# Kernel tuning notes

Hardware: AMD Instinct MI355X
Metric: run time of the kernel (lower is better)

## Reference

```python
import jax, jax.numpy as jnp
import numpy as np

HEADS = 4
DIM_HEAD = 128
HIDDEN = HEADS * DIM_HEAD  # 512
DIM = 256
EMBED = 256


def mish(x):
    return x * jnp.tanh(jax.nn.softplus(x))


def setup_inputs() -> dict:
    key = jax.random.key(0)
    k = jax.random.split(key, 7)
    b, a, f, t = 64, 8, DIM, 256
    x = jax.random.normal(k[0], (b, a, f, t), dtype=jnp.float32)
    time = jax.random.normal(k[1], (b, a, EMBED), dtype=jnp.float32)
    # to_qkv: Conv2d(dim, 3*hidden, 1, bias=False) -> weight [3*hidden, dim]
    w_qkv = jax.random.normal(k[2], (3 * HIDDEN, DIM), dtype=jnp.float32) * (1.0 / np.sqrt(DIM))
    # time_mlp: Mish -> Linear(embed, 3*hidden)
    w_time = jax.random.normal(k[3], (3 * HIDDEN, EMBED), dtype=jnp.float32) * (1.0 / np.sqrt(EMBED))
    b_time = jax.random.normal(k[4], (3 * HIDDEN,), dtype=jnp.float32) * 0.01
    # to_out: Conv2d(hidden, dim, 1) with bias
    w_out = jax.random.normal(k[5], (DIM, HIDDEN), dtype=jnp.float32) * (1.0 / np.sqrt(HIDDEN))
    b_out = jax.random.normal(k[6], (DIM,), dtype=jnp.float32) * 0.01
    return {"x": x, "time": time, "w_qkv": w_qkv, "w_time": w_time,
            "b_time": b_time, "w_out": w_out, "b_out": b_out}


def reference(x, time, w_qkv, w_time, b_time, w_out, b_out):
    b, a, f, t = x.shape
    heads, c = HEADS, DIM_HEAD
    # x: b a f t -> b f a t (channels-first for 1x1 conv)
    xp = jnp.transpose(x, (0, 2, 1, 3))  # [b, f, a, t]
    # 1x1 conv == channel GEMM
    qkv = jnp.einsum('of,bfat->boat', w_qkv, xp)  # [b, 3*hidden, a, t]
    # time MLP: Mish -> Linear; bias broadcast over t
    temb = mish(time) @ w_time.T + b_time          # [b, a, 3*hidden]
    temb = jnp.transpose(temb, (0, 2, 1))[..., None]  # [b, 3*hidden, a, 1]
    qkv = qkv + temb
    # 'b (qkv heads c) h w -> qkv (b h) heads c w' with h=a, w=t
    qkv = qkv.reshape(b, 3, heads, c, a, t)
    qkv = jnp.transpose(qkv, (1, 0, 4, 2, 3, 5)).reshape(3, b * a, heads, c, t)
    q, k, v = qkv[0], qkv[1], qkv[2]  # each [(b a), heads, c, t]
    k = jax.nn.softmax(k, axis=-1)
    # linear attention: context over keys/values, then apply to q
    context = jnp.einsum('bhdn,bhen->bhde', k, v)   # [(b a), heads, c, c]
    out = jnp.einsum('bhde,bhdn->bhen', context, q)  # [(b a), heads, c, t]
    # '(b h) heads c w -> b (heads c) h w'
    out = out.reshape(b, a, heads * c, t)
    out = jnp.transpose(out, (0, 2, 1, 3))  # [b, hidden, a, t]
    out = jnp.einsum('of,bfat->boat', w_out, out) + b_out[None, :, None, None]
    # b f a t -> b a f t
    return jnp.transpose(out, (0, 2, 1, 3))
```

## Files before the change

kernel.cpp:

```cpp
#include <hip/hip_runtime.h>

typedef __bf16 bf16;
typedef __bf16 bf16x4 __attribute__((ext_vector_type(4)));
typedef __bf16 bf16x8 __attribute__((ext_vector_type(8)));
typedef float  f32x4  __attribute__((ext_vector_type(4)));

#define TT    256
#define FF    256
#define NS    512

#define TSTR  40
#define TSZ2  (128 * TSTR)

#define SCHED0 __builtin_amdgcn_sched_barrier(0)
#define BAR    __builtin_amdgcn_s_barrier()
#define WAITVM(N) asm volatile("s_waitcnt vmcnt(" #N ")" ::: "memory")
#define WAITLGKM0 asm volatile("s_waitcnt lgkmcnt(0)" ::: "memory")
#define SP1 __builtin_amdgcn_s_setprio(1)
#define SP0 __builtin_amdgcn_s_setprio(0)

static __device__ inline f32x4 mfma16(bf16x8 a, bf16x8 b, f32x4 c) {
    return __builtin_amdgcn_mfma_f32_16x16x32_bf16(a, b, c, 0, 0, 0);
}

typedef const __attribute__((address_space(1))) unsigned int* gp_t;
typedef __attribute__((address_space(3))) unsigned int* lp_t;
static __device__ inline void gll16(const bf16* g, bf16* l) {
    __builtin_amdgcn_global_load_lds((gp_t)g, (lp_t)l, 16, 0, 0);
}


static __device__ inline void stage128g(const bf16* __restrict__ g, int ld, bf16* __restrict__ l) {
    int lane = threadIdx.x & 63, wv = threadIdx.x >> 6;
    int r = lane >> 2;
    int c8 = ((lane & 3) ^ ((lane >> 3) & 3)) * 8;
#pragma unroll
    for (int i = 0; i < 2; i++) {
        int row0 = wv * 32 + i * 16;
        gll16(g + (size_t)(row0 + r) * ld + c8, l + row0 * 32);
    }
}
static __device__ inline void stage8(const bf16* __restrict__ g, int ld, bf16* __restrict__ l) {
    int lane = threadIdx.x & 63, wv = threadIdx.x >> 6;
    int r = lane >> 2;
    int c8 = ((lane & 3) ^ ((lane >> 3) & 3)) * 8;
    int row0 = wv * 16;
    gll16(g + (size_t)(row0 + r) * ld + c8, l + row0 * 32);
}
static __device__ inline bf16x8 fragld(const bf16* __restrict__ l, int row0) {
    int lane = threadIdx.x & 63;
    int r15 = lane & 15;
    int kg = (lane >> 4) ^ ((r15 >> 1) & 3);
    return *(const bf16x8*)(l + (row0 + r15) * 32 + kg * 8);
}
static __device__ inline bf16x8 fragld_s(const bf16* __restrict__ l, int row0, int stride) {
    int lane = threadIdx.x & 63;
    return *(const bf16x8*)(l + (row0 + (lane & 15)) * stride + (lane >> 4) * 8);
}

__global__ __launch_bounds__(256) void k_cvt(const float4* __restrict__ src, bf16* __restrict__ dst) {
    int i = blockIdx.x * 256 + threadIdx.x;
    float4 v = src[i];
    bf16x4 o;
    o[0] = (__bf16)v.x; o[1] = (__bf16)v.y; o[2] = (__bf16)v.z; o[3] = (__bf16)v.w;
    *(bf16x4*)(dst + (size_t)i * 4) = o;
}

__global__ __launch_bounds__(256) void k_mish(const float4* __restrict__ src, bf16* __restrict__ dst) {
    int i = blockIdx.x * 256 + threadIdx.x;
    float4 v = src[i];
    float in[4] = {v.x, v.y, v.z, v.w};
    bf16x4 o;
#pragma unroll
    for (int j = 0; j < 4; j++) {
        float sp = log1pf(__expf(in[j]));
        o[j] = (__bf16)(in[j] * tanhf(sp));
    }
    *(bf16x4*)(dst + (size_t)i * 4) = o;
}

__global__ __launch_bounds__(256) void k_xpose(const float* __restrict__ x, bf16* __restrict__ xT) {
    __shared__ float tile[64][65];
    int bid = blockIdx.x;
    int s  = bid >> 4;
    int f0 = ((bid >> 2) & 3) * 64;
    int t0 = (bid & 3) * 64;
    int tid = threadIdx.x;
    int rr = tid >> 4;
    int cc = (tid & 15) * 4;
    const float* xp = x + ((size_t)(s * FF + f0)) * TT + t0;
#pragma unroll
    for (int i = 0; i < 4; i++) {
        int r = i * 16 + rr;
        float4 v = *(const float4*)(xp + (size_t)r * TT + cc);
        tile[r][cc] = v.x; tile[r][cc + 1] = v.y; tile[r][cc + 2] = v.z; tile[r][cc + 3] = v.w;
    }
    __syncthreads();
    bf16* op = xT + ((size_t)(s * TT + t0)) * FF + f0;
#pragma unroll
    for (int i = 0; i < 4; i++) {
        int tr = i * 16 + rr;
        bf16x4 o;
        o[0] = (__bf16)tile[cc][tr];     o[1] = (__bf16)tile[cc + 1][tr];
        o[2] = (__bf16)tile[cc + 2][tr]; o[3] = (__bf16)tile[cc + 3][tr];
        *(bf16x4*)(op + (size_t)tr * FF + cc) = o;
    }
}

__global__ __launch_bounds__(256) void k_temb(const bf16* __restrict__ wt, const bf16* __restrict__ mish,
                                              const float* __restrict__ bt, float* __restrict__ tembT) {
    __shared__ bf16 lA[128 * 32];
    __shared__ bf16 lB[128 * 32];
    int o0 = blockIdx.x * 128, s0 = blockIdx.y * 128;
    int tid = threadIdx.x, wv = tid >> 6, lane = tid & 63, qd = lane >> 4, c = lane & 15;
    f32x4 acc[2][8] = {};
    for (int k0 = 0; k0 < 256; k0 += 32) {
        __syncthreads();
        stage128g(wt + (size_t)o0 * 256 + k0, 256, lA);
        stage128g(mish + (size_t)s0 * 256 + k0, 256, lB);
        __syncthreads();
        bf16x8 a0 = fragld(lA, wv * 32), a1 = fragld(lA, wv * 32 + 16);
#pragma unroll
        for (int nt = 0; nt < 8; nt++) {
            bf16x8 b = fragld(lB, nt * 16);
            acc[0][nt] = mfma16(a0, b, acc[0][nt]);
            acc[1][nt] = mfma16(a1, b, acc[1][nt]);
        }
    }
#pragma unroll
    for (int mt = 0; mt < 2; mt++)
#pragma unroll
        for (int nt = 0; nt < 8; nt++)
#pragma unroll
            for (int r = 0; r < 4; r++) {
                int o = o0 + wv * 32 + mt * 16 + qd * 4 + r;
                int s = s0 + nt * 16 + c;
                tembT[(size_t)o * 512 + s] = acc[mt][nt][r] + bt[o];
            }
}

#define LXF(i)  ((bf16*)(smem + (size_t)(i) * 8192))
#define LWAF(i) ((bf16*)(smem + 24576 + (size_t)(i) * 8192))
#define LWBF(i) ((bf16*)(smem + 49152 + (size_t)(i) * 8192))
#define KV_STAGE(st) { int _b = (st) % 3; stage8(xh + (st) * 32, 256, LXF(_b)); \
                       stage8(Wk + (st) * 32, 256, LWAF(_b)); stage8(Wv + (st) * 32, 256, LWBF(_b)); }
#define Q_STAGE(st)  { int _b = (st) % 3; stage8(xh2 + (st) * 32, 256, LXF(_b)); \
                       stage8(Wq + (st) * 32, 256, LWAF(_b)); }
__global__ __launch_bounds__(512, 2) void k_fused(const bf16* __restrict__ wqkv, const bf16* __restrict__ xT,
                                                  const float* __restrict__ tembT, bf16* __restrict__ midT) {
    __shared__ __align__(16) char smem[156160];
    float* ls  = (float*)(smem + 73728);
    bf16*  lk  = (bf16*)(smem + 74240);
    bf16*  lct = (bf16*)(smem + 74240);
    bf16*  lv  = (bf16*)(smem + 115200);
    bf16*  lq  = (bf16*)(smem + 115200);

    int b = blockIdx.x;
    int w = (b & 7) * (4 * NS / 8) + (b >> 3);
    int s = w >> 2, h = w & 3;
    int tid = threadIdx.x, wv = tid >> 6, lane = tid & 63, qd = lane >> 4, c = lane & 15;
    int wa = wv >> 1;
    int wb = wv & 1;
    const bf16* xs = xT + (size_t)s * (TT * FF);
    const bf16* Wq = wqkv + (size_t)(h * 128) * 256;
    const bf16* Wk = wqkv + (size_t)(512 + h * 128) * 256;
    const bf16* Wv = wqkv + (size_t)(1024 + h * 128) * 256;

    if (tid < 128) ls[tid] = 0.f;

    f32x4 cacc[2][4] = {};

    float tbk2[4], tbv2[4];
#pragma unroll
    for (int nt = 0; nt < 4; nt++) {
        int ch = wb * 64 + nt * 16 + c;
        tbk2[nt] = tembT[(size_t)(512 + h * 128 + ch) * 512 + s];
        tbv2[nt] = tembT[(size_t)(1024 + h * 128 + ch) * 512 + s];
    }

    for (int th = 0; th < 2; th++) {
        f32x4 kacc[2][4] = {}, vacc[2][4] = {};
        const bf16* xh = xs + (size_t)th * 128 * 256;
        KV_STAGE(0); SCHED0; KV_STAGE(1); SCHED0; KV_STAGE(2); SCHED0;
#pragma unroll
        for (int p = 0; p < 4; p++) {
            if (p == 3) { WAITVM(0); } else { WAITVM(3); }
            SCHED0; BAR; SCHED0;
            SP1;
#pragma unroll
            for (int u = 0; u < 2; u++) {
                int tb = (2 * p + u) % 3;
                bf16x8 a0 = fragld(LXF(tb), wa * 32);
                bf16x8 a1 = fragld(LXF(tb), wa * 32 + 16);
#pragma unroll
                for (int nt = 0; nt < 4; nt++) {
                    int row = wb * 64 + nt * 16;
                    bf16x8 bk = fragld(LWAF(tb), row);
                    bf16x8 bv = fragld(LWBF(tb), row);
                    kacc[0][nt] = mfma16(a0, bk, kacc[0][nt]);
                    kacc[1][nt] = mfma16(a1, bk, kacc[1][nt]);
                    vacc[0][nt] = mfma16(a0, bv, vacc[0][nt]);
                    vacc[1][nt] = mfma16(a1, bv, vacc[1][nt]);
                }
            }
            SP0;
            SCHED0; BAR; SCHED0;
            if (p == 0) { KV_STAGE(3); KV_STAGE(4); }
            else if (p == 1) { KV_STAGE(5); KV_STAGE(6); }
            else if (p == 2) { KV_STAGE(7); }
            SCHED0;
        }
        {
#pragma unroll
            for (int nt = 0; nt < 4; nt++) {
                int ch = wb * 64 + nt * 16 + c;
                float ps = 0.f;
                bf16x4 ok0, ok1, ov0, ov1;
#pragma unroll
                for (int r = 0; r < 4; r++) {
                    bf16 e0 = (__bf16)__expf(kacc[0][nt][r] + tbk2[nt]);
                    bf16 e1 = (__bf16)__expf(kacc[1][nt][r] + tbk2[nt]);
                    ok0[r] = e0; ok1[r] = e1; ps += (float)e0 + (float)e1;
                    ov0[r] = (__bf16)(vacc[0][nt][r] + tbv2[nt]);
                    ov1[r] = (__bf16)(vacc[1][nt][r] + tbv2[nt]);
                }
                int ad = wa * TSZ2 + ch * TSTR + qd * 4;
                *(bf16x4*)(lk + ad)      = ok0;
                *(bf16x4*)(lk + ad + 16) = ok1;
                *(bf16x4*)(lv + ad)      = ov0;
                *(bf16x4*)(lv + ad + 16) = ov1;
                ps += __shfl_xor(ps, 16);
                ps += __shfl_xor(ps, 32);
                if (qd == 0) atomicAdd(&ls[ch], ps);
            }
        }
        __syncthreads();
        SP1;
#pragma unroll
        for (int tc = 0; tc < 4; tc++) {
            bf16x8 a0 = fragld_s(lv + tc * TSZ2, wa * 32, TSTR);
            bf16x8 a1 = fragld_s(lv + tc * TSZ2, wa * 32 + 16, TSTR);
#pragma unroll
            for (int nt = 0; nt < 4; nt++) {
                bf16x8 kf = fragld_s(lk + tc * TSZ2, wb * 64 + nt * 16, TSTR);
                cacc[0][nt] = mfma16(a0, kf, cacc[0][nt]);
                cacc[1][nt] = mfma16(a1, kf, cacc[1][nt]);
            }
        }
        SP0;
        __syncthreads();
    }

    {
        const bf16* xh2 = xs;
        Q_STAGE(0); SCHED0; Q_STAGE(1); SCHED0; Q_STAGE(2); SCHED0;
    }

#pragma unroll
    for (int ai = 0; ai < 2; ai++)
#pragma unroll
        for (int nt = 0; nt < 4; nt++) {
            int d = wb * 64 + nt * 16 + c;
            float rv = 1.0f / ls[d];
#pragma unroll
            for (int r = 0; r < 4; r++)
                lct[(wa * 32 + ai * 16 + qd * 4 + r) * 136 + d] = (__bf16)(cacc[ai][nt][r] * rv);
        }
    WAITLGKM0;
    SCHED0; BAR; SCHED0;

    float tbq2[2][4];
#pragma unroll
    for (int ai = 0; ai < 2; ai++)
#pragma unroll
        for (int r = 0; r < 4; r++)
            tbq2[ai][r] = tembT[(size_t)(h * 128 + wa * 32 + ai * 16 + qd * 4 + r) * 512 + s];
    for (int th = 0; th < 2; th++) {
        f32x4 qacc[2][4] = {};
        const bf16* xh2 = xs + (size_t)th * 128 * 256;
        if (th == 1) { Q_STAGE(0); SCHED0; Q_STAGE(1); SCHED0; Q_STAGE(2); SCHED0; }
#pragma unroll
        for (int p = 0; p < 4; p++) {
            if (p == 3) { WAITVM(0); } else { WAITVM(2); }
            SCHED0; BAR; SCHED0;
            SP1;
#pragma unroll
            for (int u = 0; u < 2; u++) {
                int tb = (2 * p + u) % 3;
                bf16x8 a0 = fragld(LWAF(tb), wa * 32);
                bf16x8 a1 = fragld(LWAF(tb), wa * 32 + 16);
#pragma unroll
                for (int nt = 0; nt < 4; nt++) {
                    bf16x8 xf = fragld(LXF(tb), wb * 64 + nt * 16);
                    qacc[0][nt] = mfma16(a0, xf, qacc[0][nt]);
                    qacc[1][nt] = mfma16(a1, xf, qacc[1][nt]);
                }
            }
            SP0;
            SCHED0; BAR; SCHED0;
            if (p == 0) { Q_STAGE(3); Q_STAGE(4); }
            else if (p == 1) { Q_STAGE(5); Q_STAGE(6); }
            else if (p == 2) { Q_STAGE(7); }
            SCHED0;
        }
        {
#pragma unroll
            for (int nt = 0; nt < 4; nt++) {
                int t = wb * 64 + nt * 16 + c;
#pragma unroll
                for (int ai = 0; ai < 2; ai++) {
                    bf16x4 oq;
#pragma unroll
                    for (int r = 0; r < 4; r++) oq[r] = (__bf16)(qacc[ai][nt][r] + tbq2[ai][r]);
                    *(bf16x4*)(lq + wa * TSZ2 + t * TSTR + ai * 16 + qd * 4) = oq;
                }
            }
        }
        __syncthreads();
        f32x4 oacc[2][4] = {};
        SP1;
#pragma unroll
        for (int dd = 0; dd < 4; dd++) {
            bf16x8 a0 = fragld_s(lct + dd * 32, wa * 32, 136);
            bf16x8 a1 = fragld_s(lct + dd * 32, wa * 32 + 16, 136);
#pragma unroll
            for (int nt = 0; nt < 4; nt++) {
                bf16x8 qf = fragld_s(lq + dd * TSZ2, wb * 64 + nt * 16, TSTR);
                oacc[0][nt] = mfma16(a0, qf, oacc[0][nt]);
                oacc[1][nt] = mfma16(a1, qf, oacc[1][nt]);
            }
        }
        SP0;
#pragma unroll
        for (int nt = 0; nt < 4; nt++)
#pragma unroll
            for (int ai = 0; ai < 2; ai++) {
                int t = th * 128 + wb * 64 + nt * 16 + c;
                int e = wa * 32 + ai * 16 + qd * 4;
                bf16x4 o;
#pragma unroll
                for (int r = 0; r < 4; r++) o[r] = (__bf16)oacc[ai][nt][r];
                *(bf16x4*)(midT + ((size_t)s * 256 + t) * 512 + h * 128 + e) = o;
            }
        __syncthreads();
    }
}

__global__ __launch_bounds__(256) void k_out(const bf16* __restrict__ wo, const bf16* __restrict__ midT,
                                             const float* __restrict__ bo, float* __restrict__ y) {
    __shared__ bf16 lA[3][128 * 32];
    __shared__ bf16 lB[3][128 * 32];
    int b = blockIdx.x;
    int w = (b & 7) * (4 * NS / 8) + (b >> 3);
    int s = w >> 2, j = w & 3;
    int o0 = (j >> 1) * 128, t0 = (j & 1) * 128;
    int tid = threadIdx.x, wv = tid >> 6, lane = tid & 63, qd = lane >> 4, c = lane & 15;
    const bf16* wA = wo + (size_t)o0 * 512;
    const bf16* ms = midT + (size_t)s * 131072 + (size_t)t0 * 512;
    f32x4 acc[2][8] = {};
    stage128g(wA, 512, lA[0]);       stage128g(ms, 512, lB[0]);       SCHED0;
    stage128g(wA + 32, 512, lA[1]);  stage128g(ms + 32, 512, lB[1]);  SCHED0;
    stage128g(wA + 64, 512, lA[2]);  stage128g(ms + 64, 512, lB[2]);  SCHED0;
#pragma unroll
    for (int p = 0; p < 8; p++) {
        if (p == 7) { WAITVM(0); } else { WAITVM(4); }
        SCHED0; BAR; SCHED0;
        SP1;
#pragma unroll
        for (int u = 0; u < 2; u++) {
            int tb = (2 * p + u) % 3;
            bf16x8 a0 = fragld(lA[tb], wv * 32), a1 = fragld(lA[tb], wv * 32 + 16);
#pragma unroll
            for (int nt = 0; nt < 8; nt++) {
                bf16x8 bfr = fragld(lB[tb], nt * 16);
                acc[0][nt] = mfma16(a0, bfr, acc[0][nt]);
                acc[1][nt] = mfma16(a1, bfr, acc[1][nt]);
            }
        }
        SP0;
        SCHED0; BAR; SCHED0;
        {
            int s1 = 2 * p + 3;
            if (s1 < 16)     { stage128g(wA + s1 * 32, 512, lA[s1 % 3]);
                               stage128g(ms + s1 * 32, 512, lB[s1 % 3]); }
            if (s1 + 1 < 16) { stage128g(wA + (s1 + 1) * 32, 512, lA[(s1 + 1) % 3]);
                               stage128g(ms + (s1 + 1) * 32, 512, lB[(s1 + 1) % 3]); }
        }
        SCHED0;
    }
    float bb[2][4];
#pragma unroll
    for (int mt = 0; mt < 2; mt++)
#pragma unroll
        for (int r = 0; r < 4; r++)
            bb[mt][r] = bo[o0 + wv * 32 + mt * 16 + qd * 4 + r];
#pragma unroll
    for (int mt = 0; mt < 2; mt++)
#pragma unroll
        for (int nt = 0; nt < 8; nt++)
#pragma unroll
            for (int r = 0; r < 4; r++) {
                int o = o0 + wv * 32 + mt * 16 + qd * 4 + r;
                int t = t0 + nt * 16 + c;
                y[((size_t)(s * 256 + o)) * 256 + t] = acc[mt][nt][r] + bb[mt][r];
            }
}

extern "C" void kernel_launch(void* const* d_in, const int* in_sizes, int n_in,
                              void* d_out, int out_size, void* d_ws, size_t ws_size,
                              hipStream_t stream) {
    const float* x      = (const float*)d_in[0];
    const float* time_  = (const float*)d_in[1];
    const float* w_qkv  = (const float*)d_in[2];
    const float* w_time = (const float*)d_in[3];
    const float* b_time = (const float*)d_in[4];
    const float* w_out  = (const float*)d_in[5];
    const float* b_out  = (const float*)d_in[6];
    float* y = (float*)d_out;
    char* ws = (char*)d_ws;

    bf16*  wqkv_bf  = (bf16*)(ws + 0);
    bf16*  wtime_bf = (bf16*)(ws + 786432);
    bf16*  wout_bf  = (bf16*)(ws + 1572864);
    bf16*  mish_bf  = (bf16*)(ws + 1835008);
    float* tembT    = (float*)(ws + 2097152);
    bf16*  xT       = (bf16*)(ws + 5242880);
    bf16*  midT     = (bf16*)(ws + 72351744);

    k_cvt<<<384, 256, 0, stream>>>((const float4*)w_qkv, wqkv_bf);
    k_cvt<<<384, 256, 0, stream>>>((const float4*)w_time, wtime_bf);
    k_cvt<<<128, 256, 0, stream>>>((const float4*)w_out, wout_bf);
    k_mish<<<128, 256, 0, stream>>>((const float4*)time_, mish_bf);
    k_temb<<<dim3(12, 4), 256, 0, stream>>>(wtime_bf, mish_bf, b_time, tembT);

    k_xpose<<<NS * 16, 256, 0, stream>>>(x, xT);
    k_fused<<<NS * 4, 512, 0, stream>>>(wqkv_bf, xT, tembT, midT);
    k_out<<<NS * 4, 256, 0, stream>>>(wout_bf, midT, b_out, y);
}
```

Baseline: 551.4 us.

## Widen k_out tiles to cover all 256 output channels per block

The output projection kernel now uses 512-thread blocks that each compute all 256 output channels for a 128-wide t tile, instead of 256-thread blocks computing 128x128 tiles. Each midT tile is therefore loaded once rather than twice, and each wave computes a 64x64 sub-tile for better fragment reuse. This halves the grid size and raises LDS use per block, which may lower occupancy and depends on stage128g/stage8 covering the new tile shapes correctly.

After: 556.6 us. No clear change (+0.9%).

```diff
diff --git a/kernel.cpp b/kernel.cpp
--- a/kernel.cpp
+++ b/kernel.cpp
@@ -346,63 +346,66 @@
     }
 }
 
-__global__ __launch_bounds__(256) void k_out(const bf16* __restrict__ wo, const bf16* __restrict__ midT,
-                                             const float* __restrict__ bo, float* __restrict__ y) {
-    __shared__ bf16 lA[3][128 * 32];
+__global__ __launch_bounds__(512, 4) void k_out(const bf16* __restrict__ wo, const bf16* __restrict__ midT,
+                                                const float* __restrict__ bo, float* __restrict__ y) {
+    __shared__ bf16 lA[3][256 * 32];
     __shared__ bf16 lB[3][128 * 32];
     int b = blockIdx.x;
-    int w = (b & 7) * (4 * NS / 8) + (b >> 3);
-    int s = w >> 2, j = w & 3;
-    int o0 = (j >> 1) * 128, t0 = (j & 1) * 128;
+    int w = (b & 7) * (2 * NS / 8) + (b >> 3);
+    int s = w >> 1, t0 = (w & 1) * 128;
     int tid = threadIdx.x, wv = tid >> 6, lane = tid & 63, qd = lane >> 4, c = lane & 15;
-    const bf16* wA = wo + (size_t)o0 * 512;
+    int wa = wv >> 1;
+    int wb = wv & 1;
     const bf16* ms = midT + (size_t)s * 131072 + (size_t)t0 * 512;
-    f32x4 acc[2][8] = {};
-    stage128g(wA, 512, lA[0]);       stage128g(ms, 512, lB[0]);       SCHED0;
-    stage128g(wA + 32, 512, lA[1]);  stage128g(ms + 32, 512, lB[1]);  SCHED0;
-    stage128g(wA + 64, 512, lA[2]);  stage128g(ms + 64, 512, lB[2]);  SCHED0;
+    f32x4 acc[4][4] = {};
+    stage128g(wo, 512, lA[0]);      stage8(ms, 512, lB[0]);      SCHED0;
+    stage128g(wo + 32, 512, lA[1]); stage8(ms + 32, 512, lB[1]); SCHED0;
+    stage128g(wo + 64, 512, lA[2]); stage8(ms + 64, 512, lB[2]); SCHED0;
 #pragma unroll
     for (int p = 0; p < 8; p++) {
-        if (p == 7) { WAITVM(0); } else { WAITVM(4); }
+        if (p == 7) { WAITVM(0); } else { WAITVM(3); }
         SCHED0; BAR; SCHED0;
         SP1;
 #pragma unroll
         for (int u = 0; u < 2; u++) {
             int tb = (2 * p + u) % 3;
-            bf16x8 a0 = fragld(lA[tb], wv * 32), a1 = fragld(lA[tb], wv * 32 + 16);
-#pragma unroll
-            for (int nt = 0; nt < 8; nt++) {
-                bf16x8 bfr = fragld(lB[tb], nt * 16);
-                acc[0][nt] = mfma16(a0, bfr, acc[0][nt]);
-                acc[1][nt] = mfma16(a1, bfr, acc[1][nt]);
+            bf16x8 a[4];
+#pragma unroll
+            for (int ai = 0; ai < 4; ai++) a[ai] = fragld(lA[tb], wa * 64 + ai * 16);
+#pragma unroll
+            for (int nt = 0; nt < 4; nt++) {
+                bf16x8 bfr = fragld(lB[tb], wb * 64 + nt * 16);
+#pragma unroll
+                for (int ai = 0; ai < 4; ai++)
+                    acc[ai][nt] = mfma16(a[ai], bfr, acc[ai][nt]);
             }
         }
         SP0;
         SCHED0; BAR; SCHED0;
         {
             int s1 = 2 * p + 3;
-            if (s1 < 16)     { stage128g(wA + s1 * 32, 512, lA[s1 % 3]);
-                               stage128g(ms + s1 * 32, 512, lB[s1 % 3]); }
-            if (s1 + 1 < 16) { stage128g(wA + (s1 + 1) * 32, 512, lA[(s1 + 1) % 3]);
-                               stage128g(ms + (s1 + 1) * 32, 512, lB[(s1 + 1) % 3]); }
+            if (s1 < 16)     { stage128g(wo + s1 * 32, 512, lA[s1 % 3]);
+                               stage8(ms + s1 * 32, 512, lB[s1 % 3]); }
+            if (s1 + 1 < 16) { stage128g(wo + (s1 + 1) * 32, 512, lA[(s1 + 1) % 3]);
+                               stage8(ms + (s1 + 1) * 32, 512, lB[(s1 + 1) % 3]); }
         }
         SCHED0;
     }
-    float bb[2][4];
-#pragma unroll
-    for (int mt = 0; mt < 2; mt++)
+    float bb[4][4];
+#pragma unroll
+    for (int ai = 0; ai < 4; ai++)
 #pragma unroll
         for (int r = 0; r < 4; r++)
-            bb[mt][r] = bo[o0 + wv * 32 + mt * 16 + qd * 4 + r];
-#pragma unroll
-    for (int mt = 0; mt < 2; mt++)
-#pragma unroll
-        for (int nt = 0; nt < 8; nt++)
+            bb[ai][r] = bo[wa * 64 + ai * 16 + qd * 4 + r];
+#pragma unroll
+    for (int ai = 0; ai < 4; ai++)
+#pragma unroll
+        for (int nt = 0; nt < 4; nt++)
 #pragma unroll
             for (int r = 0; r < 4; r++) {
-                int o = o0 + wv * 32 + mt * 16 + qd * 4 + r;
-                int t = t0 + nt * 16 + c;
-                y[((size_t)(s * 256 + o)) * 256 + t] = acc[mt][nt][r] + bb[mt][r];
+                int o = wa * 64 + ai * 16 + qd * 4 + r;
+                int t = t0 + wb * 64 + nt * 16 + c;
+                y[((size_t)(s * 256 + o)) * 256 + t] = acc[ai][nt][r] + bb[ai][r];
             }
 }
 
@@ -435,5 +438,5 @@
 
     k_xpose<<<NS * 16, 256, 0, stream>>>(x, xT);
     k_fused<<<NS * 4, 512, 0, stream>>>(wqkv_bf, xT, tembT, midT);
-    k_out<<<NS * 4, 256, 0, stream>>>(wout_bf, midT, b_out, y);
-}
+    k_out<<<2 * NS, 512, 0, stream>>>(wout_bf, midT, b_out, y);
+}
```

## Shrink fused kernel LDS footprint to fit two blocks per CU

Applied to the files above, without the earlier changes.

Repacks the fused attention kernel's shared memory from about 156 KB to 76.8 KB so two 512-thread blocks can be resident per CU. It overlaps the K/V/Q/context tiles with the staging buffers, narrows the padded tile stride from 40 to 36, and cuts the Q-projection staging from triple to double buffering with a simpler per-step prefetch. Launch bounds now ask for 4 waves per EU, which caps VGPRs at 128 and may cause spills. The shallower Q pipeline and the new stride may also change latency hiding and LDS bank conflicts.

After: 727.5 us. +31.9%, slower.

```diff
diff --git a/kernel.cpp b/kernel.cpp
--- a/kernel.cpp
+++ b/kernel.cpp
@@ -9,8 +9,8 @@
 #define FF    256
 #define NS    512
 
-#define TSTR  40
-#define TSZ2  (128 * TSTR)
+#define TSTR3 36
+#define TSZ3  (128 * TSTR3)
 
 #define SCHED0 __builtin_amdgcn_sched_barrier(0)
 #define BAR    __builtin_amdgcn_s_barrier()
@@ -139,21 +139,23 @@
             }
 }
 
-#define LXF(i)  ((bf16*)(smem + (size_t)(i) * 8192))
-#define LWAF(i) ((bf16*)(smem + 24576 + (size_t)(i) * 8192))
-#define LWBF(i) ((bf16*)(smem + 49152 + (size_t)(i) * 8192))
+#define LXF(i)   ((bf16*)(smem + (size_t)(i) * 8192))
+#define LWAF(i)  ((bf16*)(smem + 24576 + (size_t)(i) * 8192))
+#define LWBF(i)  ((bf16*)(smem + 49152 + (size_t)(i) * 8192))
+#define LXF2(i)  ((bf16*)(smem + (size_t)(i) * 8192))
+#define LWAF2(i) ((bf16*)(smem + 16384 + (size_t)(i) * 8192))
 #define KV_STAGE(st) { int _b = (st) % 3; stage8(xh + (st) * 32, 256, LXF(_b)); \
                        stage8(Wk + (st) * 32, 256, LWAF(_b)); stage8(Wv + (st) * 32, 256, LWBF(_b)); }
-#define Q_STAGE(st)  { int _b = (st) % 3; stage8(xh2 + (st) * 32, 256, LXF(_b)); \
-                       stage8(Wq + (st) * 32, 256, LWAF(_b)); }
-__global__ __launch_bounds__(512, 2) void k_fused(const bf16* __restrict__ wqkv, const bf16* __restrict__ xT,
+#define Q_STAGE2(st) { int _b = (st) & 1; stage8(xh2 + (st) * 32, 256, LXF2(_b)); \
+                       stage8(Wq + (st) * 32, 256, LWAF2(_b)); }
+__global__ __launch_bounds__(512, 4) void k_fused(const bf16* __restrict__ wqkv, const bf16* __restrict__ xT,
                                                   const float* __restrict__ tembT, bf16* __restrict__ midT) {
-    __shared__ __align__(16) char smem[156160];
-    float* ls  = (float*)(smem + 73728);
-    bf16*  lk  = (bf16*)(smem + 74240);
-    bf16*  lct = (bf16*)(smem + 74240);
-    bf16*  lv  = (bf16*)(smem + 115200);
-    bf16*  lq  = (bf16*)(smem + 115200);
+    __shared__ __align__(16) char smem[76800];
+    bf16*  lk  = (bf16*)(smem);
+    bf16*  lv  = (bf16*)(smem + 36864);
+    bf16*  lct = (bf16*)(smem + 40960);
+    bf16*  lq  = (bf16*)(smem);
+    float* ls  = (float*)(smem + 76288);
 
     int b = blockIdx.x;
     int w = (b & 7) * (4 * NS / 8) + (b >> 3);
@@ -224,7 +226,7 @@
                     ov0[r] = (__bf16)(vacc[0][nt][r] + tbv2[nt]);
                     ov1[r] = (__bf16)(vacc[1][nt][r] + tbv2[nt]);
                 }
-                int ad = wa * TSZ2 + ch * TSTR + qd * 4;
+                int ad = wa * TSZ3 + ch * TSTR3 + qd * 4;
                 *(bf16x4*)(lk + ad)      = ok0;
                 *(bf16x4*)(lk + ad + 16) = ok1;
                 *(bf16x4*)(lv + ad)      = ov0;
@@ -238,11 +240,11 @@
         SP1;
 #pragma unroll
         for (int tc = 0; tc < 4; tc++) {
-            bf16x8 a0 = fragld_s(lv + tc * TSZ2, wa * 32, TSTR);
-            bf16x8 a1 = fragld_s(lv + tc * TSZ2, wa * 32 + 16, TSTR);
+            bf16x8 a0 = fragld_s(lv + tc * TSZ3, wa * 32, TSTR3);
+            bf16x8 a1 = fragld_s(lv + tc * TSZ3, wa * 32 + 16, TSTR3);
 #pragma unroll
             for (int nt = 0; nt < 4; nt++) {
-                bf16x8 kf = fragld_s(lk + tc * TSZ2, wb * 64 + nt * 16, TSTR);
+                bf16x8 kf = fragld_s(lk + tc * TSZ3, wb * 64 + nt * 16, TSTR3);
                 cacc[0][nt] = mfma16(a0, kf, cacc[0][nt]);
                 cacc[1][nt] = mfma16(a1, kf, cacc[1][nt]);
             }
@@ -253,7 +255,7 @@
 
     {
         const bf16* xh2 = xs;
-        Q_STAGE(0); SCHED0; Q_STAGE(1); SCHED0; Q_STAGE(2); SCHED0;
+        Q_STAGE2(0); SCHED0; Q_STAGE2(1); SCHED0;
     }
 
 #pragma unroll
@@ -278,29 +280,25 @@
     for (int th = 0; th < 2; th++) {
         f32x4 qacc[2][4] = {};
         const bf16* xh2 = xs + (size_t)th * 128 * 256;
-        if (th == 1) { Q_STAGE(0); SCHED0; Q_STAGE(1); SCHED0; Q_STAGE(2); SCHED0; }
-#pragma unroll
-        for (int p = 0; p < 4; p++) {
-            if (p == 3) { WAITVM(0); } else { WAITVM(2); }
+        if (th == 1) { Q_STAGE2(0); SCHED0; Q_STAGE2(1); SCHED0; }
+#pragma unroll
+        for (int t = 0; t < 8; t++) {
+            if (t == 7) { WAITVM(0); } else { WAITVM(2); }
             SCHED0; BAR; SCHED0;
             SP1;
-#pragma unroll
-            for (int u = 0; u < 2; u++) {
-                int tb = (2 * p + u) % 3;
-                bf16x8 a0 = fragld(LWAF(tb), wa * 32);
-                bf16x8 a1 = fragld(LWAF(tb), wa * 32 + 16);
+            {
+                bf16x8 a0 = fragld(LWAF2(t & 1), wa * 32);
+                bf16x8 a1 = fragld(LWAF2(t & 1), wa * 32 + 16);
 #pragma unroll
                 for (int nt = 0; nt < 4; nt++) {
-                    bf16x8 xf = fragld(LXF(tb), wb * 64 + nt * 16);
+                    bf16x8 xf = fragld(LXF2(t & 1), wb * 64 + nt * 16);
                     qacc[0][nt] = mfma16(a0, xf, qacc[0][nt]);
                     qacc[1][nt] = mfma16(a1, xf, qacc[1][nt]);
                 }
             }
             SP0;
             SCHED0; BAR; SCHED0;
-            if (p == 0) { Q_STAGE(3); Q_STAGE(4); }
-            else if (p == 1) { Q_STAGE(5); Q_STAGE(6); }
-            else if (p == 2) { Q_STAGE(7); }
+            if (t + 2 < 8) { Q_STAGE2(t + 2); }
             SCHED0;
         }
         {
@@ -312,7 +310,7 @@
                     bf16x4 oq;
 #pragma unroll
                     for (int r = 0; r < 4; r++) oq[r] = (__bf16)(qacc[ai][nt][r] + tbq2[ai][r]);
-                    *(bf16x4*)(lq + wa * TSZ2 + t * TSTR + ai * 16 + qd * 4) = oq;
+                    *(bf16x4*)(lq + wa * TSZ3 + t * TSTR3 + ai * 16 + qd * 4) = oq;
                 }
             }
         }
@@ -325,7 +323,7 @@
             bf16x8 a1 = fragld_s(lct + dd * 32, wa * 32 + 16, 136);
 #pragma unroll
             for (int nt = 0; nt < 4; nt++) {
-                bf16x8 qf = fragld_s(lq + dd * TSZ2, wb * 64 + nt * 16, TSTR);
+                bf16x8 qf = fragld_s(lq + dd * TSZ3, wb * 64 + nt * 16, TSTR3);
                 oacc[0][nt] = mfma16(a0, qf, oacc[0][nt]);
                 oacc[1][nt] = mfma16(a1, qf, oacc[1][nt]);
             }
@@ -435,5 +433,5 @@
 
     k_xpose<<<NS * 16, 256, 0, stream>>>(x, xT);
     k_fused<<<NS * 4, 512, 0, stream>>>(wqkv_bf, xT, tembT, midT);
-    k_out<<<NS * 4, 256, 0, stream>>>(wout_bf, midT, b_out, y);
-}
+    k_out<<<4 * NS, 256, 0, stream>>>(wout_bf, midT, b_out, y);
+}
```
